# Optimization experiments

Measured on AMD Instinct MI355X. Metric: run time of the kernel, lower is better.

## Reference

```python
import jax, jax.numpy as jnp
import numpy as np

B, T, R, D = 32, 128, 49, 512
H_EXP, H_CLS = 256, 256
THRES = 0.1
LAM = 4.0
NEG_INF = -1e9


def setup_inputs() -> dict:
    key = jax.random.key(0)
    ks = jax.random.split(key, 16)
    s = 0.02
    return {
        "word_emb": jax.random.normal(ks[0], (B, T, D), jnp.float32),
        "region_emb": jax.random.normal(ks[1], (B, R, D), jnp.float32),
        "attention_mask": jnp.ones((B, T), jnp.int32),
        # pos expert MLP: D -> H_EXP -> 1
        "pw1": jax.random.normal(ks[2], (D, H_EXP), jnp.float32) * s,
        "pb1": jnp.zeros((H_EXP,), jnp.float32),
        "pw2": jax.random.normal(ks[3], (H_EXP, 1), jnp.float32) * s,
        "pb2": jnp.zeros((1,), jnp.float32),
        # neg expert MLP: D -> H_EXP -> 1
        "nw1": jax.random.normal(ks[4], (D, H_EXP), jnp.float32) * s,
        "nb1": jnp.zeros((H_EXP,), jnp.float32),
        "nw2": jax.random.normal(ks[5], (H_EXP, 1), jnp.float32) * s,
        "nb2": jnp.zeros((1,), jnp.float32),
        # fc: D -> 1
        "fcw": jax.random.normal(ks[6], (D, 1), jnp.float32) * s,
        "fcb": jnp.zeros((1,), jnp.float32),
        # classifier: D -> H_CLS -> 2 (dropout is eval-mode identity)
        "cw1": jax.random.normal(ks[7], (D, H_CLS), jnp.float32) * s,
        "cb1": jnp.zeros((H_CLS,), jnp.float32),
        "cw2": jax.random.normal(ks[8], (H_CLS, 2), jnp.float32) * s,
        "cb2": jnp.zeros((2,), jnp.float32),
    }


def _mlp_score(x, w1, b1, w2, b2):
    # sigmoid(Linear(tanh(Linear(x)))) -> squeeze last dim
    return jax.nn.sigmoid(jnp.tanh(x @ w1 + b1) @ w2 + b2)[..., 0]


def reference(word_emb, region_emb, attention_mask,
              pw1, pb1, pw2, pb2, nw1, nb1, nw2, nb2,
              fcw, fcb, cw1, cb1, cw2, cb2):
    mask_f = attention_mask.astype(word_emb.dtype)  # [B,T]

    # cross attention word x region: [B,T,R]
    attn = jnp.einsum("btd,brd->btr", word_emb, region_emb)
    attn_neg = (attn - THRES > 0).astype(attn.dtype)  # [B,T,R]
    attn_pos = jax.nn.softmax(
        jnp.where(attn_neg > 0, attn, NEG_INF) * LAM, axis=-1)
    pos = jnp.einsum("btr,brd->btd", attn_pos, region_emb) + word_emb

    # pos expert: sigmoid score, zeroed where token has no positive region
    # or is padding (padding tokens were excluded by the ragged gather).
    expert_neg_mask = attn_neg.sum(-1) == 0  # [B,T] bool
    pos_score = _mlp_score(pos, pw1, pb1, pw2, pb2)  # [B,T]
    pos_score = jnp.where(expert_neg_mask, 0.0, pos_score) * mask_f
    pos_score = jax.nn.relu(pos_score)
    pos_agg = jnp.einsum("bt,btd->bd", pos_score, pos)

    # neg expert over all (token, region) pair embeddings, masked to the
    # ragged set neg_mask = (1 - attn_neg) * attention_mask
    all_emb = word_emb[:, :, None, :] + region_emb[:, None, :, :]  # [B,T,R,D]
    neg_mask = (1.0 - attn_neg) * mask_f[:, :, None]  # [B,T,R]
    neg_score = _mlp_score(all_emb, nw1, nb1, nw2, nb2)  # [B,T,R]
    neg_score = jax.nn.relu(neg_score * neg_mask)
    neg_agg = jnp.einsum("btr,btrd->bd", neg_score, all_emb)

    result = jnp.stack([neg_agg, pos_agg], axis=1)  # [B,2,D]

    choose = (result @ fcw + fcb)[..., 0]  # [B,2]
    choose_mask = attn_neg.sum(axis=(-1, -2)) == 0  # [B]
    choose = choose.at[:, 0].set(
        jnp.where(choose_mask, NEG_INF, choose[:, 0]))
    path_prob = jax.nn.softmax(choose, axis=-1)  # [B,2]
    final = jnp.einsum("bk,bkd->bd", path_prob, result)  # [B,D]

    logits = jax.nn.relu(final @ cw1 + cb1) @ cw2 + cb2  # [B,2]
    return (logits, path_prob)
```

## Files before the change

kernel.cpp:

```cpp
#include <hip/hip_runtime.h>

#define B_ 32
#define T_ 128
#define R_ 49
#define D_ 512
#define HE_ 256
#define HC_ 256

#define NG_PACK 64
#define NG_K1 512
#define NG_G1 177
#define NG_G2 128
#define NG_NEGB 512

typedef float f32x4 __attribute__((ext_vector_type(4)));
typedef short s16x8 __attribute__((ext_vector_type(8)));
typedef short s16x4 __attribute__((ext_vector_type(4)));

__device__ __forceinline__ unsigned short bf16rne(float f) {
  unsigned u = __float_as_uint(f);
  u += 0x7FFF + ((u >> 16) & 1);
  return (unsigned short)(u >> 16);
}
__device__ __forceinline__ float rcp_fast(float x) {
  return __builtin_amdgcn_rcpf(x);
}
__device__ __forceinline__ float tanh_fast(float x) {
  float e = __expf(2.0f * x);
  return fmaf(-2.0f, rcp_fast(e + 1.0f), 1.0f);
}
__device__ __forceinline__ float sigmoid_fast(float x) {
  return rcp_fast(1.0f + __expf(-x));
}
__device__ __forceinline__ float wave_sum(float v) {
#pragma unroll
  for (int off = 32; off; off >>= 1) v += __shfl_down(v, off);
  return v;
}

__global__ __launch_bounds__(512, 4) void k1_pack(
    const float* __restrict__ word, const float* __restrict__ region,
    const float* __restrict__ nw1, const float* __restrict__ pw1,
    const int* __restrict__ amask, unsigned short* __restrict__ wp,
    float* __restrict__ pos, float* __restrict__ negcnt,
    unsigned long long* __restrict__ nmask) {
  __shared__ float attn_s[8][52];
  __shared__ alignas(16) float wp_T[49][8];
  int tid = threadIdx.x, wave = tid >> 6, lane = tid & 63;
  int bid = blockIdx.x;

  if (bid < NG_PACK) {
    int gid = bid * 512 + tid;
    int mat = gid >> 14;
    int rem = gid & 16383;
    int plane = rem & 63;
    int tile = rem >> 6;
    int kt = tile >> 4, ct = tile & 15;
    const float* W = mat ? pw1 : nw1;
    int k0 = kt * 32 + (plane >> 4) * 8;
    int c = ct * 16 + (plane & 15);
    s16x8 pk;
#pragma unroll
    for (int j = 0; j < 8; ++j)
      pk[j] = (short)bf16rne(W[(size_t)(k0 + j) * HE_ + c]);
    *(s16x8*)(wp + (size_t)gid * 8) = pk;
    return;
  }

  int bid2 = bid - NG_PACK;
  int b = bid2 >> 4;
  int t0 = (bid2 & 15) * 8;
  int bt0 = b * T_ + t0;
  const float* reg = region + (size_t)b * R_ * D_;
  const float4* word4 = (const float4*)word;
  int il = lane & 15, g = lane >> 4;

  float4 wv[2][8];
#pragma unroll
  for (int q = 0; q < 2; ++q)
#pragma unroll
    for (int kq = 0; kq < 8; ++kq)
      wv[q][kq] = word4[(size_t)(bt0 + q * 4 + g) * 128 + il + kq * 16];

  for (int r = wave; r < R_; r += 8) {
    const float4* rrow4 = (const float4*)(reg + (size_t)r * D_);
    float4 rv[8];
#pragma unroll
    for (int kq = 0; kq < 8; ++kq) rv[kq] = rrow4[il + kq * 16];
#pragma unroll
    for (int q = 0; q < 2; ++q) {
      float acc = 0.f;
#pragma unroll
      for (int kq = 0; kq < 8; ++kq) {
        float4 w = wv[q][kq], rr = rv[kq];
        acc = fmaf(w.x, rr.x, acc);
        acc = fmaf(w.y, rr.y, acc);
        acc = fmaf(w.z, rr.z, acc);
        acc = fmaf(w.w, rr.w, acc);
      }
      acc += __shfl_xor(acc, 8);
      acc += __shfl_xor(acc, 4);
      acc += __shfl_xor(acc, 2);
      acc += __shfl_xor(acc, 1);
      if (il == 0) attn_s[q * 4 + g][r] = acc;
    }
  }
  __syncthreads();

  {
    int t = wave;
    int am = amask[bt0 + t];
    float a = (lane < R_) ? attn_s[t][lane] : 0.f;
    float neg = (lane < R_ && (a - 0.1f) > 0.f) ? 1.f : 0.f;
    float masked = (lane < R_) ? ((neg > 0.f) ? a * 4.0f : -4e9f) : -3.0e38f;
    float cnt = wave_sum(neg);
    float m = masked;
#pragma unroll
    for (int off = 32; off; off >>= 1) m = fmaxf(m, __shfl_down(m, off));
    m = __shfl(m, 0);
    float e = (lane < R_) ? __expf(masked - m) : 0.f;
    float s = wave_sum(e);
    s = __shfl(s, 0);
    if (lane < R_) wp_T[lane][t] = e / s;
    bool want = (lane < R_) && (neg == 0.f) && (am != 0);
    unsigned long long bm = __ballot(want);
    if (lane == 0) {
      negcnt[bt0 + t] = cnt;
      nmask[bt0 + t] = bm;
    }
  }
  __syncthreads();

  int d = tid;
  float accs[8] = {0.f, 0.f, 0.f, 0.f, 0.f, 0.f, 0.f, 0.f};
#pragma unroll 7
  for (int r = 0; r < R_; ++r) {
    float gg = reg[(size_t)r * D_ + d];
    float4 w0 = *(const float4*)&wp_T[r][0];
    float4 w1 = *(const float4*)&wp_T[r][4];
    accs[0] = fmaf(w0.x, gg, accs[0]);
    accs[1] = fmaf(w0.y, gg, accs[1]);
    accs[2] = fmaf(w0.z, gg, accs[2]);
    accs[3] = fmaf(w0.w, gg, accs[3]);
    accs[4] = fmaf(w1.x, gg, accs[4]);
    accs[5] = fmaf(w1.y, gg, accs[5]);
    accs[6] = fmaf(w1.z, gg, accs[6]);
    accs[7] = fmaf(w1.w, gg, accs[7]);
  }
#pragma unroll
  for (int t = 0; t < 8; ++t) {
    size_t base = (size_t)(bt0 + t) * D_ + d;
    pos[base] = word[base] + accs[t];
  }
}

__global__ __launch_bounds__(512) void gemm_all(
    const float* __restrict__ word, const float* __restrict__ region,
    const float* __restrict__ pos, const unsigned short* __restrict__ wpack,
    const float* __restrict__ nb1, const float* __restrict__ pb1,
    const float* __restrict__ pw2, const float* __restrict__ pb2,
    const float* __restrict__ negcnt, const int* __restrict__ amask,
    float* __restrict__ wh, float* __restrict__ rh,
    float* __restrict__ pscore) {
  __shared__ alignas(16) unsigned short As[32 * 512];
  __shared__ float sred[32][4];
  int tid = threadIdx.x, wave = tid >> 6, lane = tid & 63;
  int bid = blockIdx.x;

  bool isg2 = (bid >= NG_G1);
  const float* A;
  float* outp = nullptr;
  int row0;
  bool useb = false;
  const s16x8* Wp8;
  if (!isg2) {
    if (bid < 128) {
      A = word; outp = wh; row0 = bid * 32; useb = true;
    } else {
      A = region; outp = rh; row0 = (bid - 128) * 32;
    }
    Wp8 = (const s16x8*)wpack;
  } else {
    A = pos; row0 = (bid - NG_G1) * 32;
    Wp8 = (const s16x8*)wpack + 16384;
  }
  const float4* A4 = (const float4*)(A + (size_t)row0 * D_);
#pragma unroll
  for (int it = 0; it < 8; ++it) {
    int f = it * 512 + tid;
    int row = f >> 7, kq = f & 127;
    float4 v = A4[f];
    int bo = (row * 1024 + kq * 8) ^ ((row & 7) << 4);
    s16x4 pk;
    pk[0] = (short)bf16rne(v.x);
    pk[1] = (short)bf16rne(v.y);
    pk[2] = (short)bf16rne(v.z);
    pk[3] = (short)bf16rne(v.w);
    *(s16x4*)((char*)As + bo) = pk;
  }
  __syncthreads();
  int rl = lane & 15, kg = lane >> 4;
  int ct0 = wave, ct1 = wave + 8;
  f32x4 acc[2][2];
#pragma unroll
  for (int s = 0; s < 2; ++s)
#pragma unroll
    for (int ci = 0; ci < 2; ++ci) acc[s][ci] = (f32x4){0.f, 0.f, 0.f, 0.f};
#pragma unroll
  for (int kt = 0; kt < 16; ++kt) {
    s16x8 b0 = Wp8[(size_t)(kt * 16 + ct0) * 64 + lane];
    s16x8 b1 = Wp8[(size_t)(kt * 16 + ct1) * 64 + lane];
#pragma unroll
    for (int sub = 0; sub < 2; ++sub) {
      int bo = ((sub * 16 + rl) * 1024 + kt * 64 + kg * 16) ^ ((rl & 7) << 4);
      s16x8 af = *(const s16x8*)((char*)As + bo);
      acc[sub][0] = __builtin_amdgcn_mfma_f32_16x16x32_bf16(af, b0, acc[sub][0], 0, 0, 0);
      acc[sub][1] = __builtin_amdgcn_mfma_f32_16x16x32_bf16(af, b1, acc[sub][1], 0, 0, 0);
    }
  }
  if (!isg2) {
    float bb0 = useb ? nb1[ct0 * 16 + rl] : 0.f;
    float bb1 = useb ? nb1[ct1 * 16 + rl] : 0.f;
#pragma unroll
    for (int sub = 0; sub < 2; ++sub) {
      int r0 = row0 + sub * 16 + kg * 4;
#pragma unroll
      for (int q = 0; q < 4; ++q) {
        outp[(size_t)(r0 + q) * HE_ + ct0 * 16 + rl] = acc[sub][0][q] + bb0;
        outp[(size_t)(r0 + q) * HE_ + ct1 * 16 + rl] = acc[sub][1][q] + bb1;
      }
    }
    return;
  }
  __syncthreads();
  float* hp_s = (float*)As;
#pragma unroll
  for (int sub = 0; sub < 2; ++sub)
#pragma unroll
    for (int q = 0; q < 4; ++q) {
      hp_s[(sub * 16 + kg * 4 + q) * 256 + ct0 * 16 + rl] = acc[sub][0][q];
      hp_s[(sub * 16 + kg * 4 + q) * 256 + ct1 * 16 + rl] = acc[sub][1][q];
    }
  __syncthreads();
  int c = tid & 255, jh = tid >> 8;
  float pb1c = pb1[c], pw2c = pw2[c];
#pragma unroll
  for (int jj = 0; jj < 16; ++jj) {
    int j = jh * 16 + jj;
    float v = tanh_fast(hp_s[j * 256 + c] + pb1c) * pw2c;
    v = wave_sum(v);
    if (lane == 0) sred[j][wave & 3] = v;
  }
  __syncthreads();
  if (tid < 32) {
    float s = sred[tid][0] + sred[tid][1] + sred[tid][2] + sred[tid][3] +
              pb2[0];
    s = sigmoid_fast(s);
    int row = row0 + tid;
    if (negcnt[row] == 0.f) s = 0.f;
    s *= (float)amask[row];
    pscore[row] = fmaxf(s, 0.f);
  }
}

__global__ __launch_bounds__(512, 6) void neg_expert(
    const float* __restrict__ wh, const float* __restrict__ rh,
    const float* __restrict__ nw2, const float* __restrict__ nb2,
    const unsigned long long* __restrict__ nmask, float* __restrict__ nst,
    float* __restrict__ nsr_sl) {
  __shared__ alignas(16) float rh_s[R_ * HE_];
  __shared__ int plist[400];
  __shared__ float nst_l[8];
  __shared__ float nsr_l[52];
  __shared__ int cnt_s[8];
  __shared__ int off_s[8];
  __shared__ int P_s;
  int tid = threadIdx.x, wave = tid >> 6, lane = tid & 63;
  int nb = blockIdx.x;
  int b = nb >> 4, t0 = (nb & 15) * 8;
  int bt0 = b * T_ + t0;
  {
    const float4* src = (const float4*)(rh + (size_t)b * R_ * HE_);
    float4* dst = (float4*)rh_s;
    for (int i = tid; i < R_ * (HE_ / 4); i += 512) dst[i] = src[i];
  }
  if (tid < 8) {
    nst_l[tid] = 0.f;
    cnt_s[tid] = __popcll(nmask[bt0 + tid]);
  }
  if (tid < R_) nsr_l[tid] = 0.f;
  __syncthreads();
  if (tid == 0) {
    int tot = 0;
#pragma unroll
    for (int w = 0; w < 8; ++w) {
      off_s[w] = tot;
      tot += cnt_s[w];
    }
    P_s = tot;
  }
  __syncthreads();
  {
    unsigned long long mw = nmask[bt0 + wave];
    if (lane < R_ && ((mw >> lane) & 1ull)) {
      int pfx = __popcll(mw & ((1ull << lane) - 1ull));
      plist[off_s[wave] + pfx] = (wave << 6) | lane;
    }
  }
  __syncthreads();
  int P = P_s;
  int grp = tid >> 4, gl = tid & 15;
  float4 wnr[4];
#pragma unroll
  for (int k = 0; k < 4; ++k)
    wnr[k] = ((const float4*)nw2)[4 * gl + ((gl + k) & 3)];
  float bias = nb2[0];
  for (int i = grp; i < P; i += 32) {
    int tr = plist[i];
    int t = tr >> 6, r = tr & 63;
    const float4* wrow = (const float4*)(wh + (size_t)(bt0 + t) * HE_);
    const float4* rrow = (const float4*)(rh_s + r * HE_);
    float acc = 0.f;
#pragma unroll
    for (int k = 0; k < 4; ++k) {
      int c = 4 * gl + ((gl + k) & 3);
      float4 hw = wrow[c];
      float4 hr = rrow[c];
      float4 wn = wnr[k];
      acc = fmaf(tanh_fast(hw.x + hr.x), wn.x, acc);
      acc = fmaf(tanh_fast(hw.y + hr.y), wn.y, acc);
      acc = fmaf(tanh_fast(hw.z + hr.z), wn.z, acc);
      acc = fmaf(tanh_fast(hw.w + hr.w), wn.w, acc);
    }
    acc += __shfl_xor(acc, 1);
    acc += __shfl_xor(acc, 2);
    acc += __shfl_xor(acc, 4);
    acc += __shfl_xor(acc, 8);
    if (gl == 0) {
      float s = sigmoid_fast(acc + bias);
      atomicAdd(&nst_l[t], s);
      atomicAdd(&nsr_l[r], s);
    }
  }
  __syncthreads();
  if (tid < 8) {
    nst[bt0 + tid] = nst_l[tid];
  } else if (tid >= 64 && tid < 64 + R_) {
    nsr_sl[(size_t)nb * R_ + (tid - 64)] = nsr_l[tid - 64];
  }
}

__global__ __launch_bounds__(512) void k7a_agg(
    const float* __restrict__ word, const float* __restrict__ region,
    const float* __restrict__ pos, const float* __restrict__ pscore,
    const float* __restrict__ nst, const float* __restrict__ nsr_sl,
    float* __restrict__ nagg, float* __restrict__ pagg) {
  int b = blockIdx.x >> 3, dc = blockIdx.x & 7;
  int tid = threadIdx.x;
  int dl = tid & 63, ts = tid >> 6;
  int d = dc * 64 + dl;
  __shared__ float nst_s[T_], psc_s[T_], nsr_s[R_];
  __shared__ float redn[8][64], redp[8][64];
  if (tid < T_) {
    psc_s[tid] = pscore[b * T_ + tid];
    nst_s[tid] = nst[b * T_ + tid];
  } else if (tid < T_ + R_) {
    int r = tid - T_;
    float s = 0.f;
#pragma unroll
    for (int tt = 0; tt < 16; ++tt)
      s += nsr_sl[(size_t)(b * 16 + tt) * R_ + r];
    nsr_s[r] = s;
  }
  __syncthreads();
  float na = 0.f, pa = 0.f;
  for (int t = ts; t < T_; t += 8) {
    size_t base = ((size_t)(b * T_ + t)) * D_ + d;
    na = fmaf(nst_s[t], word[base], na);
    pa = fmaf(psc_s[t], pos[base], pa);
  }
  for (int r = ts; r < R_; r += 8)
    na = fmaf(nsr_s[r], region[((size_t)(b * R_ + r)) * D_ + d], na);
  redn[ts][dl] = na;
  redp[ts][dl] = pa;
  __syncthreads();
  if (tid < 64) {
    float s = 0.f;
#pragma unroll
    for (int k = 0; k < 8; ++k) s += redn[k][tid];
    nagg[(size_t)b * D_ + dc * 64 + tid] = s;
  } else if (tid < 128) {
    int l = tid - 64;
    float s = 0.f;
#pragma unroll
    for (int k = 0; k < 8; ++k) s += redp[k][l];
    pagg[(size_t)b * D_ + dc * 64 + l] = s;
  }
}

__global__ __launch_bounds__(256) void k7b_tail(
    const float* __restrict__ nagg, const float* __restrict__ pagg,
    const float* __restrict__ negcnt, const float* __restrict__ fcw,
    const float* __restrict__ fcb, const float* __restrict__ cw1,
    const float* __restrict__ cb1, const float* __restrict__ cw2,
    const float* __restrict__ cb2, float* __restrict__ out) {
  int b = blockIdx.x, tid = threadIdx.x, lane = tid & 63, wave = tid >> 6;
  __shared__ float na_s[D_], pa_s[D_], fin[D_];
  __shared__ float red[8];
  __shared__ float pp0, pp1;
  float cntp = (tid < T_) ? negcnt[b * T_ + tid] : 0.f;
  float cw = wave_sum(cntp);
  if (lane == 0) red[wave] = cw;
  int d0 = tid, d1 = tid + 256;
  float n0 = nagg[(size_t)b * D_ + d0], n1 = nagg[(size_t)b * D_ + d1];
  float p0 = pagg[(size_t)b * D_ + d0], p1 = pagg[(size_t)b * D_ + d1];
  na_s[d0] = n0;
  na_s[d1] = n1;
  pa_s[d0] = p0;
  pa_s[d1] = p1;
  __syncthreads();
  float cnt_total = red[0] + red[1] + red[2] + red[3];
  float f0 = fcw[d0], f1 = fcw[d1];
  float c0p = n0 * f0 + n1 * f1;
  float c1p = p0 * f0 + p1 * f1;
  c0p = wave_sum(c0p);
  c1p = wave_sum(c1p);
  __syncthreads();
  if (lane == 0) { red[wave] = c0p; red[wave + 4] = c1p; }
  __syncthreads();
  if (tid == 0) {
    float c0 = red[0] + red[1] + red[2] + red[3] + fcb[0];
    float c1 = red[4] + red[5] + red[6] + red[7] + fcb[0];
    if (cnt_total == 0.f) c0 = -1e9f;
    float m = fmaxf(c0, c1);
    float e0 = __expf(c0 - m), e1 = __expf(c1 - m);
    float inv = 1.f / (e0 + e1);
    pp0 = e0 * inv;
    pp1 = e1 * inv;
    out[2 * B_ + 2 * b + 0] = pp0;
    out[2 * B_ + 2 * b + 1] = pp1;
  }
  __syncthreads();
  for (int d = tid; d < D_; d += 256) fin[d] = pp0 * na_s[d] + pp1 * pa_s[d];
  __syncthreads();
  float a0 = cb1[tid], a1 = 0.f, a2 = 0.f, a3 = 0.f;
#pragma unroll 4
  for (int d = 0; d < D_; d += 4) {
    a0 = fmaf(fin[d + 0], cw1[(size_t)(d + 0) * HC_ + tid], a0);
    a1 = fmaf(fin[d + 1], cw1[(size_t)(d + 1) * HC_ + tid], a1);
    a2 = fmaf(fin[d + 2], cw1[(size_t)(d + 2) * HC_ + tid], a2);
    a3 = fmaf(fin[d + 3], cw1[(size_t)(d + 3) * HC_ + tid], a3);
  }
  float acc = fmaxf((a0 + a1) + (a2 + a3), 0.f);
  float l0 = acc * cw2[2 * tid + 0];
  float l1 = acc * cw2[2 * tid + 1];
  l0 = wave_sum(l0);
  l1 = wave_sum(l1);
  __syncthreads();
  if (lane == 0) { red[wave] = l0; red[wave + 4] = l1; }
  __syncthreads();
  if (tid == 0) {
    out[2 * b + 0] = red[0] + red[1] + red[2] + red[3] + cb2[0];
    out[2 * b + 1] = red[4] + red[5] + red[6] + red[7] + cb2[1];
  }
}

extern "C" void kernel_launch(void* const* d_in, const int* in_sizes, int n_in,
                              void* d_out, int out_size, void* d_ws,
                              size_t ws_size, hipStream_t stream) {
  const float* word = (const float*)d_in[0];
  const float* region = (const float*)d_in[1];
  const int* amask = (const int*)d_in[2];
  const float* pw1 = (const float*)d_in[3];
  const float* pb1 = (const float*)d_in[4];
  const float* pw2 = (const float*)d_in[5];
  const float* pb2 = (const float*)d_in[6];
  const float* nw1 = (const float*)d_in[7];
  const float* nb1 = (const float*)d_in[8];
  const float* nw2 = (const float*)d_in[9];
  const float* nb2 = (const float*)d_in[10];
  const float* fcw = (const float*)d_in[11];
  const float* fcb = (const float*)d_in[12];
  const float* cw1 = (const float*)d_in[13];
  const float* cb1 = (const float*)d_in[14];
  const float* cw2 = (const float*)d_in[15];
  const float* cb2 = (const float*)d_in[16];
  float* out = (float*)d_out;

  unsigned short* wpack = (unsigned short*)d_ws;
  float* ws = (float*)d_ws + 131072;
  float* pos = ws;
  float* wh = pos + (size_t)B_ * T_ * D_;
  float* rh = wh + (size_t)B_ * T_ * HE_;
  float* nst = rh + (size_t)B_ * R_ * HE_;
  float* nsr_sl = nst + (size_t)B_ * T_;
  float* negcnt = nsr_sl + (size_t)B_ * 16 * R_;
  float* pscore = negcnt + B_ * T_;
  float* nagg = pscore + B_ * T_;
  float* pagg = nagg + (size_t)B_ * D_;
  unsigned long long* nmask =
      (unsigned long long*)(pagg + (size_t)B_ * D_);

  k1_pack<<<NG_PACK + NG_K1, 512, 0, stream>>>(
      word, region, nw1, pw1, amask, wpack, pos, negcnt, nmask);
  gemm_all<<<NG_G1 + NG_G2, 512, 0, stream>>>(
      word, region, pos, wpack, nb1, pb1, pw2, pb2, negcnt, amask, wh, rh,
      pscore);
  neg_expert<<<NG_NEGB, 512, 0, stream>>>(wh, rh, nw2, nb2, nmask, nst,
                                          nsr_sl);
  k7a_agg<<<B_ * 8, 512, 0, stream>>>(word, region, pos, pscore, nst, nsr_sl,
                                      nagg, pagg);
  k7b_tail<<<B_, 256, 0, stream>>>(nagg, pagg, negcnt, fcw, fcb, cw1, cb1,
                                   cw2, cb2, out);
}
```

Baseline: 75.96 us.

## Regroup kernels so independent GEMM and attention work share launches

Weight packing becomes its own small kernel. The word/region hidden GEMMs (wh, rh) now run in the same launch as the attention/pos computation, and the pos-expert GEMM runs together with the neg-expert scoring. Both pairs use a shared-memory union. This shortens the dependency chain: the neg expert no longer waits for a separate GEMM launch, and independent work runs concurrently. The costs are an extra tiny launch and heterogeneous blocks with larger shared-memory footprints, which may reduce occupancy.

After: 74.64 us (median of 2 runs). Within noise of the previous version (-1.7%).

```diff
diff --git a/kernel.cpp b/kernel.cpp
--- a/kernel.cpp
+++ b/kernel.cpp
@@ -7,11 +7,10 @@
 #define HE_ 256
 #define HC_ 256
 
-#define NG_PACK 64
+#define NG_WHRH 177
 #define NG_K1 512
-#define NG_G1 177
+#define NG_NEG 512
 #define NG_G2 128
-#define NG_NEGB 512
 
 typedef float f32x4 __attribute__((ext_vector_type(4)));
 typedef short s16x8 __attribute__((ext_vector_type(8)));
@@ -38,36 +37,103 @@
   return v;
 }
 
-__global__ __launch_bounds__(512, 4) void k1_pack(
+__global__ __launch_bounds__(256) void pack_w(
+    const float* __restrict__ nw1, const float* __restrict__ pw1,
+    unsigned short* __restrict__ wp) {
+  int gid = blockIdx.x * 256 + threadIdx.x;
+  int mat = gid >> 14;
+  int rem = gid & 16383;
+  int lane = rem & 63;
+  int tile = rem >> 6;
+  int kt = tile >> 4, ct = tile & 15;
+  const float* W = mat ? pw1 : nw1;
+  int k0 = kt * 32 + (lane >> 4) * 8;
+  int c = ct * 16 + (lane & 15);
+  s16x8 pk;
+#pragma unroll
+  for (int j = 0; j < 8; ++j)
+    pk[j] = (short)bf16rne(W[(size_t)(k0 + j) * HE_ + c]);
+  *(s16x8*)(wp + (size_t)gid * 8) = pk;
+}
+
+__global__ __launch_bounds__(512, 4) void k1_whrh(
     const float* __restrict__ word, const float* __restrict__ region,
-    const float* __restrict__ nw1, const float* __restrict__ pw1,
-    const int* __restrict__ amask, unsigned short* __restrict__ wp,
-    float* __restrict__ pos, float* __restrict__ negcnt,
-    unsigned long long* __restrict__ nmask) {
-  __shared__ float attn_s[8][52];
-  __shared__ alignas(16) float wp_T[49][8];
+    const unsigned short* __restrict__ wpack, const float* __restrict__ nb1,
+    const int* __restrict__ amask, float* __restrict__ wh,
+    float* __restrict__ rh, float* __restrict__ pos,
+    float* __restrict__ negcnt, unsigned long long* __restrict__ nmask) {
+  __shared__ union SM1 {
+    struct G {
+      alignas(16) unsigned short As[32 * 512];
+    } g;
+    struct K {
+      float attn_s[8][52];
+      alignas(16) float wp_T[49][8];
+    } k;
+  } sm;
   int tid = threadIdx.x, wave = tid >> 6, lane = tid & 63;
   int bid = blockIdx.x;
 
-  if (bid < NG_PACK) {
-    int gid = bid * 512 + tid;
-    int mat = gid >> 14;
-    int rem = gid & 16383;
-    int plane = rem & 63;
-    int tile = rem >> 6;
-    int kt = tile >> 4, ct = tile & 15;
-    const float* W = mat ? pw1 : nw1;
-    int k0 = kt * 32 + (plane >> 4) * 8;
-    int c = ct * 16 + (plane & 15);
-    s16x8 pk;
-#pragma unroll
-    for (int j = 0; j < 8; ++j)
-      pk[j] = (short)bf16rne(W[(size_t)(k0 + j) * HE_ + c]);
-    *(s16x8*)(wp + (size_t)gid * 8) = pk;
+  if (bid < NG_WHRH) {
+    const float* A;
+    float* outp;
+    int row0;
+    bool useb;
+    if (bid < 128) {
+      A = word; outp = wh; row0 = bid * 32; useb = true;
+    } else {
+      A = region; outp = rh; row0 = (bid - 128) * 32; useb = false;
+    }
+    const s16x8* Wp8 = (const s16x8*)wpack;
+    const float4* A4 = (const float4*)(A + (size_t)row0 * D_);
+#pragma unroll
+    for (int it = 0; it < 8; ++it) {
+      int f = it * 512 + tid;
+      int row = f >> 7, kq = f & 127;
+      float4 v = A4[f];
+      int bo = (row * 1024 + kq * 8) ^ ((row & 7) << 4);
+      s16x4 pk;
+      pk[0] = (short)bf16rne(v.x);
+      pk[1] = (short)bf16rne(v.y);
+      pk[2] = (short)bf16rne(v.z);
+      pk[3] = (short)bf16rne(v.w);
+      *(s16x4*)((char*)sm.g.As + bo) = pk;
+    }
+    __syncthreads();
+    int rl = lane & 15, kg = lane >> 4;
+    int ct0 = wave, ct1 = wave + 8;
+    f32x4 acc[2][2];
+#pragma unroll
+    for (int s = 0; s < 2; ++s)
+#pragma unroll
+      for (int ci = 0; ci < 2; ++ci) acc[s][ci] = (f32x4){0.f, 0.f, 0.f, 0.f};
+#pragma unroll
+    for (int kt = 0; kt < 16; ++kt) {
+      s16x8 b0 = Wp8[(size_t)(kt * 16 + ct0) * 64 + lane];
+      s16x8 b1 = Wp8[(size_t)(kt * 16 + ct1) * 64 + lane];
+#pragma unroll
+      for (int sub = 0; sub < 2; ++sub) {
+        int bo = ((sub * 16 + rl) * 1024 + kt * 64 + kg * 16) ^ ((rl & 7) << 4);
+        s16x8 af = *(const s16x8*)((char*)sm.g.As + bo);
+        acc[sub][0] = __builtin_amdgcn_mfma_f32_16x16x32_bf16(af, b0, acc[sub][0], 0, 0, 0);
+        acc[sub][1] = __builtin_amdgcn_mfma_f32_16x16x32_bf16(af, b1, acc[sub][1], 0, 0, 0);
+      }
+    }
+    float bb0 = useb ? nb1[ct0 * 16 + rl] : 0.f;
+    float bb1 = useb ? nb1[ct1 * 16 + rl] : 0.f;
+#pragma unroll
+    for (int sub = 0; sub < 2; ++sub) {
+      int r0 = row0 + sub * 16 + kg * 4;
+#pragma unroll
+      for (int q = 0; q < 4; ++q) {
+        outp[(size_t)(r0 + q) * HE_ + ct0 * 16 + rl] = acc[sub][0][q] + bb0;
+        outp[(size_t)(r0 + q) * HE_ + ct1 * 16 + rl] = acc[sub][1][q] + bb1;
+      }
+    }
     return;
   }
 
-  int bid2 = bid - NG_PACK;
+  int bid2 = bid - NG_WHRH;
   int b = bid2 >> 4;
   int t0 = (bid2 & 15) * 8;
   int bt0 = b * T_ + t0;
@@ -102,7 +168,7 @@
       acc += __shfl_xor(acc, 4);
       acc += __shfl_xor(acc, 2);
       acc += __shfl_xor(acc, 1);
-      if (il == 0) attn_s[q * 4 + g][r] = acc;
+      if (il == 0) sm.k.attn_s[q * 4 + g][r] = acc;
     }
   }
   __syncthreads();
@@ -110,7 +176,7 @@
   {
     int t = wave;
     int am = amask[bt0 + t];
-    float a = (lane < R_) ? attn_s[t][lane] : 0.f;
+    float a = (lane < R_) ? sm.k.attn_s[t][lane] : 0.f;
     float neg = (lane < R_ && (a - 0.1f) > 0.f) ? 1.f : 0.f;
     float masked = (lane < R_) ? ((neg > 0.f) ? a * 4.0f : -4e9f) : -3.0e38f;
     float cnt = wave_sum(neg);
@@ -121,7 +187,7 @@
     float e = (lane < R_) ? __expf(masked - m) : 0.f;
     float s = wave_sum(e);
     s = __shfl(s, 0);
-    if (lane < R_) wp_T[lane][t] = e / s;
+    if (lane < R_) sm.k.wp_T[lane][t] = e / s;
     bool want = (lane < R_) && (neg == 0.f) && (am != 0);
     unsigned long long bm = __ballot(want);
     if (lane == 0) {
@@ -136,8 +202,8 @@
 #pragma unroll 7
   for (int r = 0; r < R_; ++r) {
     float gg = reg[(size_t)r * D_ + d];
-    float4 w0 = *(const float4*)&wp_T[r][0];
-    float4 w1 = *(const float4*)&wp_T[r][4];
+    float4 w0 = *(const float4*)&sm.k.wp_T[r][0];
+    float4 w1 = *(const float4*)&sm.k.wp_T[r][4];
     accs[0] = fmaf(w0.x, gg, accs[0]);
     accs[1] = fmaf(w0.y, gg, accs[1]);
     accs[2] = fmaf(w0.z, gg, accs[2]);
@@ -154,161 +220,136 @@
   }
 }
 
-__global__ __launch_bounds__(512) void gemm_all(
-    const float* __restrict__ word, const float* __restrict__ region,
+__global__ __launch_bounds__(512, 4) void neg_g2(
     const float* __restrict__ pos, const unsigned short* __restrict__ wpack,
-    const float* __restrict__ nb1, const float* __restrict__ pb1,
-    const float* __restrict__ pw2, const float* __restrict__ pb2,
-    const float* __restrict__ negcnt, const int* __restrict__ amask,
-    float* __restrict__ wh, float* __restrict__ rh,
-    float* __restrict__ pscore) {
-  __shared__ alignas(16) unsigned short As[32 * 512];
-  __shared__ float sred[32][4];
+    const float* __restrict__ pb1, const float* __restrict__ pw2,
+    const float* __restrict__ pb2, const float* __restrict__ negcnt,
+    const int* __restrict__ amask, const float* __restrict__ wh,
+    const float* __restrict__ rh, const float* __restrict__ nw2,
+    const float* __restrict__ nb2,
+    const unsigned long long* __restrict__ nmask, float* __restrict__ pscore,
+    float* __restrict__ nst, float* __restrict__ nsr_sl) {
+  __shared__ union SM2 {
+    struct G {
+      alignas(16) unsigned short As[32 * 512];
+      float sred[32][4];
+    } g;
+    struct N {
+      alignas(16) float rh_s[R_ * HE_];
+      int plist[400];
+      float nst_l[8];
+      float nsr_l[52];
+      int cnt_s[8];
+      int off_s[8];
+      int P;
+    } n;
+  } sm;
   int tid = threadIdx.x, wave = tid >> 6, lane = tid & 63;
   int bid = blockIdx.x;
 
-  bool isg2 = (bid >= NG_G1);
-  const float* A;
-  float* outp = nullptr;
-  int row0;
-  bool useb = false;
-  const s16x8* Wp8;
-  if (!isg2) {
-    if (bid < 128) {
-      A = word; outp = wh; row0 = bid * 32; useb = true;
-    } else {
-      A = region; outp = rh; row0 = (bid - 128) * 32;
-    }
-    Wp8 = (const s16x8*)wpack;
-  } else {
-    A = pos; row0 = (bid - NG_G1) * 32;
-    Wp8 = (const s16x8*)wpack + 16384;
-  }
-  const float4* A4 = (const float4*)(A + (size_t)row0 * D_);
-#pragma unroll
-  for (int it = 0; it < 8; ++it) {
-    int f = it * 512 + tid;
-    int row = f >> 7, kq = f & 127;
-    float4 v = A4[f];
-    int bo = (row * 1024 + kq * 8) ^ ((row & 7) << 4);
-    s16x4 pk;
-    pk[0] = (short)bf16rne(v.x);
-    pk[1] = (short)bf16rne(v.y);
-    pk[2] = (short)bf16rne(v.z);
-    pk[3] = (short)bf16rne(v.w);
-    *(s16x4*)((char*)As + bo) = pk;
-  }
-  __syncthreads();
-  int rl = lane & 15, kg = lane >> 4;
-  int ct0 = wave, ct1 = wave + 8;
-  f32x4 acc[2][2];
-#pragma unroll
-  for (int s = 0; s < 2; ++s)
-#pragma unroll
-    for (int ci = 0; ci < 2; ++ci) acc[s][ci] = (f32x4){0.f, 0.f, 0.f, 0.f};
-#pragma unroll
-  for (int kt = 0; kt < 16; ++kt) {
-    s16x8 b0 = Wp8[(size_t)(kt * 16 + ct0) * 64 + lane];
-    s16x8 b1 = Wp8[(size_t)(kt * 16 + ct1) * 64 + lane];
-#pragma unroll
-    for (int sub = 0; sub < 2; ++sub) {
-      int bo = ((sub * 16 + rl) * 1024 + kt * 64 + kg * 16) ^ ((rl & 7) << 4);
-      s16x8 af = *(const s16x8*)((char*)As + bo);
-      acc[sub][0] = __builtin_amdgcn_mfma_f32_16x16x32_bf16(af, b0, acc[sub][0], 0, 0, 0);
-      acc[sub][1] = __builtin_amdgcn_mfma_f32_16x16x32_bf16(af, b1, acc[sub][1], 0, 0, 0);
-    }
-  }
-  if (!isg2) {
-    float bb0 = useb ? nb1[ct0 * 16 + rl] : 0.f;
-    float bb1 = useb ? nb1[ct1 * 16 + rl] : 0.f;
-#pragma unroll
-    for (int sub = 0; sub < 2; ++sub) {
-      int r0 = row0 + sub * 16 + kg * 4;
+  if (bid >= NG_NEG) {
+    int row0 = (bid - NG_NEG) * 32;
+    const s16x8* Wp8 = (const s16x8*)wpack + 16384;
+    const float4* A4 = (const float4*)(pos + (size_t)row0 * D_);
+#pragma unroll
+    for (int it = 0; it < 8; ++it) {
+      int f = it * 512 + tid;
+      int row = f >> 7, kq = f & 127;
+      float4 v = A4[f];
+      int bo = (row * 1024 + kq * 8) ^ ((row & 7) << 4);
+      s16x4 pk;
+      pk[0] = (short)bf16rne(v.x);
+      pk[1] = (short)bf16rne(v.y);
+      pk[2] = (short)bf16rne(v.z);
+      pk[3] = (short)bf16rne(v.w);
+      *(s16x4*)((char*)sm.g.As + bo) = pk;
+    }
+    __syncthreads();
+    int rl = lane & 15, kg = lane >> 4;
+    int ct0 = wave, ct1 = wave + 8;
+    f32x4 acc[2][2];
+#pragma unroll
+    for (int s = 0; s < 2; ++s)
+#pragma unroll
+      for (int ci = 0; ci < 2; ++ci) acc[s][ci] = (f32x4){0.f, 0.f, 0.f, 0.f};
+#pragma unroll
+    for (int kt = 0; kt < 16; ++kt) {
+      s16x8 b0 = Wp8[(size_t)(kt * 16 + ct0) * 64 + lane];
+      s16x8 b1 = Wp8[(size_t)(kt * 16 + ct1) * 64 + lane];
+#pragma unroll
+      for (int sub = 0; sub < 2; ++sub) {
+        int bo = ((sub * 16 + rl) * 1024 + kt * 64 + kg * 16) ^ ((rl & 7) << 4);
+        s16x8 af = *(const s16x8*)((char*)sm.g.As + bo);
+        acc[sub][0] = __builtin_amdgcn_mfma_f32_16x16x32_bf16(af, b0, acc[sub][0], 0, 0, 0);
+        acc[sub][1] = __builtin_amdgcn_mfma_f32_16x16x32_bf16(af, b1, acc[sub][1], 0, 0, 0);
+      }
+    }
+    __syncthreads();
+    float* hp_s = (float*)sm.g.As;
+#pragma unroll
+    for (int sub = 0; sub < 2; ++sub)
 #pragma unroll
       for (int q = 0; q < 4; ++q) {
-        outp[(size_t)(r0 + q) * HE_ + ct0 * 16 + rl] = acc[sub][0][q] + bb0;
-        outp[(size_t)(r0 + q) * HE_ + ct1 * 16 + rl] = acc[sub][1][q] + bb1;
+        hp_s[(sub * 16 + kg * 4 + q) * 256 + ct0 * 16 + rl] = acc[sub][0][q];
+        hp_s[(sub * 16 + kg * 4 + q) * 256 + ct1 * 16 + rl] = acc[sub][1][q];
       }
+    __syncthreads();
+    int c = tid & 255, jh = tid >> 8;
+    float pb1c = pb1[c], pw2c = pw2[c];
+#pragma unroll
+    for (int jj = 0; jj < 16; ++jj) {
+      int j = jh * 16 + jj;
+      float v = tanh_fast(hp_s[j * 256 + c] + pb1c) * pw2c;
+      v = wave_sum(v);
+      if (lane == 0) sm.g.sred[j][wave & 3] = v;
+    }
+    __syncthreads();
+    if (tid < 32) {
+      float s = sm.g.sred[tid][0] + sm.g.sred[tid][1] + sm.g.sred[tid][2] +
+                sm.g.sred[tid][3] + pb2[0];
+      s = sigmoid_fast(s);
+      int row = row0 + tid;
+      if (negcnt[row] == 0.f) s = 0.f;
+      s *= (float)amask[row];
+      pscore[row] = fmaxf(s, 0.f);
     }
     return;
   }
-  __syncthreads();
-  float* hp_s = (float*)As;
-#pragma unroll
-  for (int sub = 0; sub < 2; ++sub)
-#pragma unroll
-    for (int q = 0; q < 4; ++q) {
-      hp_s[(sub * 16 + kg * 4 + q) * 256 + ct0 * 16 + rl] = acc[sub][0][q];
-      hp_s[(sub * 16 + kg * 4 + q) * 256 + ct1 * 16 + rl] = acc[sub][1][q];
-    }
-  __syncthreads();
-  int c = tid & 255, jh = tid >> 8;
-  float pb1c = pb1[c], pw2c = pw2[c];
-#pragma unroll
-  for (int jj = 0; jj < 16; ++jj) {
-    int j = jh * 16 + jj;
-    float v = tanh_fast(hp_s[j * 256 + c] + pb1c) * pw2c;
-    v = wave_sum(v);
-    if (lane == 0) sred[j][wave & 3] = v;
-  }
-  __syncthreads();
-  if (tid < 32) {
-    float s = sred[tid][0] + sred[tid][1] + sred[tid][2] + sred[tid][3] +
-              pb2[0];
-    s = sigmoid_fast(s);
-    int row = row0 + tid;
-    if (negcnt[row] == 0.f) s = 0.f;
-    s *= (float)amask[row];
-    pscore[row] = fmaxf(s, 0.f);
-  }
-}
-
-__global__ __launch_bounds__(512, 6) void neg_expert(
-    const float* __restrict__ wh, const float* __restrict__ rh,
-    const float* __restrict__ nw2, const float* __restrict__ nb2,
-    const unsigned long long* __restrict__ nmask, float* __restrict__ nst,
-    float* __restrict__ nsr_sl) {
-  __shared__ alignas(16) float rh_s[R_ * HE_];
-  __shared__ int plist[400];
-  __shared__ float nst_l[8];
-  __shared__ float nsr_l[52];
-  __shared__ int cnt_s[8];
-  __shared__ int off_s[8];
-  __shared__ int P_s;
-  int tid = threadIdx.x, wave = tid >> 6, lane = tid & 63;
-  int nb = blockIdx.x;
-  int b = nb >> 4, t0 = (nb & 15) * 8;
+
+  int nb = bid;
+  int b = nb >> 4, tile = nb & 15;
+  int t0 = tile * 8;
   int bt0 = b * T_ + t0;
   {
     const float4* src = (const float4*)(rh + (size_t)b * R_ * HE_);
-    float4* dst = (float4*)rh_s;
+    float4* dst = (float4*)sm.n.rh_s;
     for (int i = tid; i < R_ * (HE_ / 4); i += 512) dst[i] = src[i];
   }
   if (tid < 8) {
-    nst_l[tid] = 0.f;
-    cnt_s[tid] = __popcll(nmask[bt0 + tid]);
-  }
-  if (tid < R_) nsr_l[tid] = 0.f;
+    sm.n.nst_l[tid] = 0.f;
+    sm.n.cnt_s[tid] = __popcll(nmask[bt0 + tid]);
+  }
+  if (tid < R_) sm.n.nsr_l[tid] = 0.f;
   __syncthreads();
   if (tid == 0) {
     int tot = 0;
 #pragma unroll
     for (int w = 0; w < 8; ++w) {
-      off_s[w] = tot;
-      tot += cnt_s[w];
-    }
-    P_s = tot;
+      sm.n.off_s[w] = tot;
+      tot += sm.n.cnt_s[w];
+    }
+    sm.n.P = tot;
   }
   __syncthreads();
   {
     unsigned long long mw = nmask[bt0 + wave];
     if (lane < R_ && ((mw >> lane) & 1ull)) {
       int pfx = __popcll(mw & ((1ull << lane) - 1ull));
-      plist[off_s[wave] + pfx] = (wave << 6) | lane;
-    }
-  }
-  __syncthreads();
-  int P = P_s;
+      sm.n.plist[sm.n.off_s[wave] + pfx] = (wave << 6) | lane;
+    }
+  }
+  __syncthreads();
+  int P = sm.n.P;
   int grp = tid >> 4, gl = tid & 15;
   float4 wnr[4];
 #pragma unroll
@@ -316,10 +357,10 @@
     wnr[k] = ((const float4*)nw2)[4 * gl + ((gl + k) & 3)];
   float bias = nb2[0];
   for (int i = grp; i < P; i += 32) {
-    int tr = plist[i];
+    int tr = sm.n.plist[i];
     int t = tr >> 6, r = tr & 63;
     const float4* wrow = (const float4*)(wh + (size_t)(bt0 + t) * HE_);
-    const float4* rrow = (const float4*)(rh_s + r * HE_);
+    const float4* rrow = (const float4*)(sm.n.rh_s + r * HE_);
     float acc = 0.f;
 #pragma unroll
     for (int k = 0; k < 4; ++k) {
@@ -338,15 +379,15 @@
     acc += __shfl_xor(acc, 8);
     if (gl == 0) {
       float s = sigmoid_fast(acc + bias);
-      atomicAdd(&nst_l[t], s);
-      atomicAdd(&nsr_l[r], s);
+      atomicAdd(&sm.n.nst_l[t], s);
+      atomicAdd(&sm.n.nsr_l[r], s);
     }
   }
   __syncthreads();
   if (tid < 8) {
-    nst[bt0 + tid] = nst_l[tid];
+    nst[bt0 + tid] = sm.n.nst_l[tid];
   } else if (tid >= 64 && tid < 64 + R_) {
-    nsr_sl[(size_t)nb * R_ + (tid - 64)] = nsr_l[tid - 64];
+    nsr_sl[(size_t)nb * R_ + (tid - 64)] = sm.n.nsr_l[tid - 64];
   }
 }
 
@@ -501,13 +542,12 @@
   unsigned long long* nmask =
       (unsigned long long*)(pagg + (size_t)B_ * D_);
 
-  k1_pack<<<NG_PACK + NG_K1, 512, 0, stream>>>(
-      word, region, nw1, pw1, amask, wpack, pos, negcnt, nmask);
-  gemm_all<<<NG_G1 + NG_G2, 512, 0, stream>>>(
-      word, region, pos, wpack, nb1, pb1, pw2, pb2, negcnt, amask, wh, rh,
-      pscore);
-  neg_expert<<<NG_NEGB, 512, 0, stream>>>(wh, rh, nw2, nb2, nmask, nst,
-                                          nsr_sl);
+  pack_w<<<128, 256, 0, stream>>>(nw1, pw1, wpack);
+  k1_whrh<<<NG_WHRH + NG_K1, 512, 0, stream>>>(
+      word, region, wpack, nb1, amask, wh, rh, pos, negcnt, nmask);
+  neg_g2<<<NG_NEG + NG_G2, 512, 0, stream>>>(
+      pos, wpack, pb1, pw2, pb2, negcnt, amask, wh, rh, nw2, nb2, nmask,
+      pscore, nst, nsr_sl);
   k7a_agg<<<B_ * 8, 512, 0, stream>>>(word, region, pos, pscore, nst, nsr_sl,
                                       nagg, pagg);
   k7b_tail<<<B_, 256, 0, stream>>>(nagg, pagg, negcnt, fcw, fcb, cw1, cb1,
```
